# Kernel tuning notes

Hardware: AMD Instinct MI355X
Metric: run time of the kernel (lower is better)

The kernel has to match this reference:

```python
import jax, jax.numpy as jnp
import numpy as np

DIM = 2048
NUM_HEADS = 16
HEAD_DIM = DIM // NUM_HEADS  # 128


def setup_inputs() -> dict:
    key = jax.random.key(0)
    ks = jax.random.split(key, 5)
    scale = 0.02
    x = jax.random.normal(ks[0], (1, 2048, DIM), dtype=jnp.float32)
    # nn.Linear weights stored as [out_features, in_features]
    Wq = jax.random.normal(ks[1], (DIM, DIM), dtype=jnp.float32) * scale
    Wk = jax.random.normal(ks[2], (HEAD_DIM, DIM), dtype=jnp.float32) * scale
    Wv = jax.random.normal(ks[3], (HEAD_DIM, DIM), dtype=jnp.float32) * scale
    Wo = jax.random.normal(ks[4], (DIM, DIM), dtype=jnp.float32) * scale
    return {"x": x, "Wq": Wq, "Wk": Wk, "Wv": Wv, "Wo": Wo}


def reference(x, Wq, Wk, Wv, Wo):
    batch, seq_len, dim = x.shape
    q = x @ Wq.T                                   # [b, s, dim]
    k = x @ Wk.T                                   # [b, s, head_dim] (shared across heads)
    v = x @ Wv.T                                   # [b, s, head_dim]
    q = q.reshape(batch, seq_len, NUM_HEADS, HEAD_DIM).transpose(0, 2, 1, 3)  # [b, h, s, d]
    # MQA: single KV head broadcast across query heads (no materialized repeat)
    scores = jnp.einsum("bhqd,bkd->bhqk", q, k) / (HEAD_DIM ** 0.5)
    probs = jax.nn.softmax(scores, axis=-1)        # [b, h, q, k]
    out = jnp.einsum("bhqk,bkd->bhqd", probs, v)   # [b, h, s, d]
    out = out.transpose(0, 2, 1, 3).reshape(batch, seq_len, dim)
    return out @ Wo.T
```

## Files before the change

kernel.cpp:

```cpp
#include <hip/hip_runtime.h>
#include <cmath>

typedef float  float4_t __attribute__((ext_vector_type(4)));
typedef __bf16 bf16x8   __attribute__((ext_vector_type(8)));
typedef unsigned short u16;

__device__ __forceinline__ u16 f2bf(float f) {
    unsigned u = __float_as_uint(f);
    u += 0x7fffu + ((u >> 16) & 1u);
    return (u16)(u >> 16);
}

#define GLOAD_LDS16(g, l)                                              \
    __builtin_amdgcn_global_load_lds(                                  \
        (__attribute__((address_space(1))) void*)(g),                  \
        (__attribute__((address_space(3))) void*)(l), 16, 0, 0)

__global__ __launch_bounds__(256) void cast_all(const float* __restrict__ x,
                                                const float* __restrict__ wq,
                                                const float* __restrict__ wk,
                                                const float* __restrict__ wv,
                                                const float* __restrict__ wo,
                                                u16* __restrict__ xb, u16* __restrict__ wqb,
                                                u16* __restrict__ wkb, u16* __restrict__ wvb,
                                                u16* __restrict__ wob) {
    const int b = blockIdx.x;
    const float* src;
    u16* dst;
    int i;
    if (b < 4096)      { src = x;  dst = xb;  i = b * 256 + threadIdx.x; }
    else if (b < 8192) { src = wq; dst = wqb; i = (b - 4096) * 256 + threadIdx.x; }
    else if (b < 8448) { src = wk; dst = wkb; i = (b - 8192) * 256 + threadIdx.x; }
    else if (b < 8704) { src = wv; dst = wvb; i = (b - 8448) * 256 + threadIdx.x; }
    else               { src = wo; dst = wob; i = (b - 8704) * 256 + threadIdx.x; }
    float4 f = ((const float4*)src)[i];
    ushort4 r;
    r.x = f2bf(f.x); r.y = f2bf(f.y); r.z = f2bf(f.z); r.w = f2bf(f.w);
    ((ushort4*)dst)[i] = r;
}

template <typename EPI>
__device__ __forceinline__ void gemm_core(const u16* __restrict__ A,
                                          const u16* __restrict__ B,
                                          int K, int bm, int bn, EPI epi) {
    __shared__ __align__(16) u16 As[2 * 64 * 32];
    __shared__ __align__(16) u16 Bs[2 * 128 * 32];
    const int tid  = threadIdx.x;
    const int lane = tid & 63, wave = tid >> 6;
    const int quad = lane >> 4, l16 = lane & 15;

    float4_t acc[4][2] = {};

    for (int k0 = 0; k0 < K; k0 += 64) {
#pragma unroll
        for (int i = 0; i < 2; ++i) {
            const int slot = i * 256 + tid;
            const int ks = slot >> 8, win = slot & 255;
            const int row = win >> 2, ch = (win & 3) * 8;
            GLOAD_LDS16(A + (size_t)(bm + row) * K + k0 + ks * 32 + ch, &As[slot * 8]);
        }
#pragma unroll
        for (int i = 0; i < 4; ++i) {
            const int slot = i * 256 + tid;
            const int ks = slot >> 9, win = slot & 511;
            const int row = win >> 2, ch = (win & 3) * 8;
            GLOAD_LDS16(B + (size_t)(bn + row) * K + k0 + ks * 32 + ch, &Bs[slot * 8]);
        }
        __syncthreads();

        bf16x8 af[2][4], bfr[2][2];
#pragma unroll
        for (int ks = 0; ks < 2; ++ks) {
#pragma unroll
            for (int mi = 0; mi < 4; ++mi)
                af[ks][mi] = *(const bf16x8*)&As[ks * 2048 + (mi * 16 + l16) * 32 + quad * 8];
#pragma unroll
            for (int ni = 0; ni < 2; ++ni)
                bfr[ks][ni] = *(const bf16x8*)&Bs[ks * 4096 + (wave * 32 + ni * 16 + l16) * 32 + quad * 8];
        }
#pragma unroll
        for (int mi = 0; mi < 4; ++mi)
#pragma unroll
            for (int ni = 0; ni < 2; ++ni) {
                acc[mi][ni] = __builtin_amdgcn_mfma_f32_16x16x32_bf16(
                    af[0][mi], bfr[0][ni], acc[mi][ni], 0, 0, 0);
                acc[mi][ni] = __builtin_amdgcn_mfma_f32_16x16x32_bf16(
                    af[1][mi], bfr[1][ni], acc[mi][ni], 0, 0, 0);
            }
        __syncthreads();
    }

#pragma unroll
    for (int mi = 0; mi < 4; ++mi) {
        const int row = bm + mi * 16 + quad * 4;
#pragma unroll
        for (int ni = 0; ni < 2; ++ni) {
            const int col = bn + wave * 32 + ni * 16 + l16;
#pragma unroll
            for (int r = 0; r < 4; ++r) epi(row + r, col, acc[mi][ni][r]);
        }
    }
}

__global__ __launch_bounds__(256) void gemm_qkv(const u16* __restrict__ A,
                                                const u16* __restrict__ B,
                                                u16* __restrict__ qb,
                                                u16* __restrict__ kb,
                                                u16* __restrict__ vtb) {
    gemm_core(A, B, 2048, blockIdx.x * 64, blockIdx.y * 128,
              [=](int row, int col, float v) {
                  if (col < 2048)
                      qb[(size_t)row * 2048 + col] = f2bf(v * 0.1275174313451427f);
                  else if (col < 2176)
                      kb[(size_t)row * 128 + (col - 2048)] = f2bf(v);
                  else
                      vtb[(size_t)(col - 2176) * 2048 + row] = f2bf(v);
              });
}

__global__ __launch_bounds__(256) void gemm_out(const u16* __restrict__ A,
                                                const u16* __restrict__ B,
                                                float* __restrict__ C) {
    gemm_core(A, B, 2048, blockIdx.x * 64, blockIdx.y * 128,
              [=](int row, int col, float v) {
                  C[(size_t)row * 2048 + col] = v;
              });
}

__global__ __launch_bounds__(256) void mqa_attn(const u16* __restrict__ Q,
                                                const u16* __restrict__ Kmat,
                                                const u16* __restrict__ Vt,
                                                float* __restrict__ Oacc0,
                                                float* __restrict__ Oacc1,
                                                float* __restrict__ Lsum) {
    __shared__ __align__(16) u16 Ks[4 * 32 * 32];
    __shared__ __align__(16) u16 Vts[128 * 32];
    __shared__ __align__(16) u16 Ps[4][32 * 40];
    const int tid  = threadIdx.x;
    const int wave = tid >> 6, lane = tid & 63;
    const int quad = lane >> 4, l16 = lane & 15;
    const int h     = blockIdx.y;
    const int ks    = blockIdx.z;
    const int qbase = blockIdx.x * 128 + wave * 32;
    const int kbase = ks * 1024;

    bf16x8 qf[2][4];
#pragma unroll
    for (int mt = 0; mt < 2; ++mt)
#pragma unroll
        for (int kb4 = 0; kb4 < 4; ++kb4)
            qf[mt][kb4] = *(const bf16x8*)(Q + (size_t)(qbase + mt * 16 + l16) * 2048 +
                                           h * 128 + kb4 * 32 + quad * 8);

    float4_t acc[2][8];
#pragma unroll
    for (int mt = 0; mt < 2; ++mt)
#pragma unroll
        for (int nt = 0; nt < 8; ++nt) acc[mt][nt] = (float4_t){0.f, 0.f, 0.f, 0.f};
    float lsum[8] = {};

    u16* pb = Ps[wave];

    for (int s = 0; s < 32; ++s) {
        const int k0 = kbase + s * 32;
#pragma unroll
        for (int i = 0; i < 2; ++i) {
            const int slot = i * 256 + tid;
            const int kb4 = slot >> 7, win = slot & 127;
            const int row = win >> 2, ch = (win & 3) * 8;
            GLOAD_LDS16(Kmat + (size_t)(k0 + row) * 128 + kb4 * 32 + ch, &Ks[slot * 8]);
        }
#pragma unroll
        for (int i = 0; i < 2; ++i) {
            const int slot = i * 256 + tid;
            const int d = slot >> 2, ch = (slot & 3) * 8;
            GLOAD_LDS16(Vt + (size_t)d * 2048 + k0 + ch, &Vts[slot * 8]);
        }
        __syncthreads();

#pragma unroll
        for (int ct = 0; ct < 2; ++ct) {
            float4_t s0 = (float4_t){0.f, 0.f, 0.f, 0.f};
            float4_t s1 = (float4_t){0.f, 0.f, 0.f, 0.f};
#pragma unroll
            for (int kb4 = 0; kb4 < 4; ++kb4) {
                bf16x8 kf = *(const bf16x8*)&Ks[kb4 * 1024 + (ct * 16 + l16) * 32 + quad * 8];
                s0 = __builtin_amdgcn_mfma_f32_16x16x32_bf16(qf[0][kb4], kf, s0, 0, 0, 0);
                s1 = __builtin_amdgcn_mfma_f32_16x16x32_bf16(qf[1][kb4], kf, s1, 0, 0, 0);
            }
#pragma unroll
            for (int r = 0; r < 4; ++r) {
                const float e0 = exp2f(s0[r]);
                const float e1 = exp2f(s1[r]);
                lsum[r]     += e0;
                lsum[4 + r] += e1;
                pb[(quad * 4 + r) * 40 + ct * 16 + l16]      = f2bf(e0);
                pb[(16 + quad * 4 + r) * 40 + ct * 16 + l16] = f2bf(e1);
            }
        }
        bf16x8 pa[2];
#pragma unroll
        for (int mt = 0; mt < 2; ++mt)
            pa[mt] = *(const bf16x8*)&pb[(mt * 16 + l16) * 40 + quad * 8];
#pragma unroll
        for (int nt = 0; nt < 8; ++nt) {
            bf16x8 vf = *(const bf16x8*)&Vts[(nt * 16 + l16) * 32 + quad * 8];
            acc[0][nt] = __builtin_amdgcn_mfma_f32_16x16x32_bf16(pa[0], vf, acc[0][nt], 0, 0, 0);
            acc[1][nt] = __builtin_amdgcn_mfma_f32_16x16x32_bf16(pa[1], vf, acc[1][nt], 0, 0, 0);
        }
        __syncthreads();
    }

    float* __restrict__ Op = ks ? Oacc1 : Oacc0;
#pragma unroll
    for (int mt = 0; mt < 2; ++mt)
#pragma unroll
        for (int r = 0; r < 4; ++r) {
            const int row = qbase + mt * 16 + quad * 4 + r;
            const size_t base = ((size_t)h * 2048 + row) * 128;
            float lrow = lsum[mt * 4 + r];
#pragma unroll
            for (int off = 1; off < 16; off <<= 1) lrow += __shfl_xor(lrow, off);
            if (l16 == 0) Lsum[(size_t)ks * 32768 + h * 2048 + row] = lrow;
#pragma unroll
            for (int nt = 0; nt < 8; ++nt)
                Op[base + nt * 16 + l16] = acc[mt][nt][r];
        }
}

__global__ __launch_bounds__(256) void attn_combine(const float* __restrict__ O0,
                                                    const float* __restrict__ O1,
                                                    const float* __restrict__ L,
                                                    u16* __restrict__ attn) {
    const int f = blockIdx.x * 256 + threadIdx.x;
    const int d4 = f & 31, h = (f >> 5) & 15, q = f >> 9;
    const int li = h * 2048 + q;
    const float inv = 1.0f / (L[li] + L[32768 + li]);
    const int oi = li * 32 + d4;
    const float4 a = ((const float4*)O0)[oi];
    const float4 b = ((const float4*)O1)[oi];
    ushort4 r;
    r.x = f2bf((a.x + b.x) * inv);
    r.y = f2bf((a.y + b.y) * inv);
    r.z = f2bf((a.z + b.z) * inv);
    r.w = f2bf((a.w + b.w) * inv);
    ((ushort4*)attn)[f] = r;
}

extern "C" void kernel_launch(void* const* d_in, const int* in_sizes, int n_in,
                              void* d_out, int out_size, void* d_ws, size_t ws_size,
                              hipStream_t stream) {
    const float* x  = (const float*)d_in[0];
    const float* Wq = (const float*)d_in[1];
    const float* Wk = (const float*)d_in[2];
    const float* Wv = (const float*)d_in[3];
    const float* Wo = (const float*)d_in[4];
    float* out = (float*)d_out;

    u16* ws   = (u16*)d_ws;
    u16* xb   = ws;
    u16* Wqb  = xb  + (4 << 20);
    u16* Wkb  = Wqb + (4 << 20);
    u16* Wvb  = Wkb + (256 << 10);
    u16* Wob  = Wvb + (256 << 10);
    u16* qb   = Wob + (4 << 20);
    u16* kb   = qb  + (4 << 20);
    u16* vtb  = kb  + (256 << 10);
    u16* attn = vtb + (256 << 10);
    float* Oacc0 = (float*)ws;
    float* Oacc1 = (float*)(attn + (4 << 20));
    float* Lsum  = Oacc1 + (4 << 20);

    cast_all<<<12800, 256, 0, stream>>>(x, Wq, Wk, Wv, Wo, xb, Wqb, Wkb, Wvb, Wob);

    gemm_qkv<<<dim3(32, 18), 256, 0, stream>>>(xb, Wqb, qb, kb, vtb);
    mqa_attn<<<dim3(16, 16, 2), 256, 0, stream>>>(qb, kb, vtb, Oacc0, Oacc1, Lsum);
    attn_combine<<<4096, 256, 0, stream>>>(Oacc0, Oacc1, Lsum, attn);
    gemm_out<<<dim3(32, 16), 256, 0, stream>>>(attn, Wob, out);
}
```

Measured before the change: 235.8 us.

## Split-K the GEMMs with 128x128 tiles and split attention keys four ways using atomics

The QKV and output GEMMs now use 128x128 block tiles over a 2x2 wave grid and split K in two across blockIdx.z. Partial results are accumulated with float atomics into zeroed buffers, and a new qkv_combine pass does the bf16 conversion, the Q scaling and the V transpose. Attention splits the key range into four chunks instead of two and accumulates O and the row sums atomically, so attn_combine reads one buffer. The aim is better tile reuse and more blocks in flight. The cost is extra memsets, atomic traffic, an extra elementwise pass and non-deterministic summation order.

```diff
diff --git a/kernel.cpp b/kernel.cpp
--- a/kernel.cpp
+++ b/kernel.cpp
@@ -40,99 +40,110 @@
 }
 
 template <typename EPI>
-__device__ __forceinline__ void gemm_core(const u16* __restrict__ A,
-                                          const u16* __restrict__ B,
-                                          int K, int bm, int bn, EPI epi) {
-    __shared__ __align__(16) u16 As[2 * 64 * 32];
-    __shared__ __align__(16) u16 Bs[2 * 128 * 32];
+__device__ __forceinline__ void gemm128_core(const u16* __restrict__ A,
+                                             const u16* __restrict__ B,
+                                             int ldk, int klen, int bm, int bn, EPI epi) {
+    __shared__ __align__(16) u16 As[128 * 32];
+    __shared__ __align__(16) u16 Bs[128 * 32];
     const int tid  = threadIdx.x;
     const int lane = tid & 63, wave = tid >> 6;
+    const int wm = wave >> 1, wn = wave & 1;
     const int quad = lane >> 4, l16 = lane & 15;
 
-    float4_t acc[4][2] = {};
-
-    for (int k0 = 0; k0 < K; k0 += 64) {
+    float4_t acc[4][4] = {};
+    const int r0 = tid >> 2;
+    const int c0 = (tid & 3) * 8;
+
+    for (int k0 = 0; k0 < klen; k0 += 32) {
 #pragma unroll
         for (int i = 0; i < 2; ++i) {
-            const int slot = i * 256 + tid;
-            const int ks = slot >> 8, win = slot & 255;
-            const int row = win >> 2, ch = (win & 3) * 8;
-            GLOAD_LDS16(A + (size_t)(bm + row) * K + k0 + ks * 32 + ch, &As[slot * 8]);
-        }
-#pragma unroll
-        for (int i = 0; i < 4; ++i) {
-            const int slot = i * 256 + tid;
-            const int ks = slot >> 9, win = slot & 511;
-            const int row = win >> 2, ch = (win & 3) * 8;
-            GLOAD_LDS16(B + (size_t)(bn + row) * K + k0 + ks * 32 + ch, &Bs[slot * 8]);
-        }
-        __syncthreads();
-
-        bf16x8 af[2][4], bfr[2][2];
-#pragma unroll
-        for (int ks = 0; ks < 2; ++ks) {
-#pragma unroll
-            for (int mi = 0; mi < 4; ++mi)
-                af[ks][mi] = *(const bf16x8*)&As[ks * 2048 + (mi * 16 + l16) * 32 + quad * 8];
-#pragma unroll
-            for (int ni = 0; ni < 2; ++ni)
-                bfr[ks][ni] = *(const bf16x8*)&Bs[ks * 4096 + (wave * 32 + ni * 16 + l16) * 32 + quad * 8];
-        }
+            const int row = i * 64 + r0;
+            const int e   = (i * 256 + tid) * 8;
+            GLOAD_LDS16(A + (size_t)(bm + row) * ldk + k0 + c0, &As[e]);
+            GLOAD_LDS16(B + (size_t)(bn + row) * ldk + k0 + c0, &Bs[e]);
+        }
+        __syncthreads();
+
+        bf16x8 af[4], bfr[4];
 #pragma unroll
         for (int mi = 0; mi < 4; ++mi)
-#pragma unroll
-            for (int ni = 0; ni < 2; ++ni) {
+            af[mi] = *(const bf16x8*)&As[(wm * 64 + mi * 16 + l16) * 32 + quad * 8];
+#pragma unroll
+        for (int ni = 0; ni < 4; ++ni)
+            bfr[ni] = *(const bf16x8*)&Bs[(wn * 64 + ni * 16 + l16) * 32 + quad * 8];
+#pragma unroll
+        for (int mi = 0; mi < 4; ++mi)
+#pragma unroll
+            for (int ni = 0; ni < 4; ++ni)
                 acc[mi][ni] = __builtin_amdgcn_mfma_f32_16x16x32_bf16(
-                    af[0][mi], bfr[0][ni], acc[mi][ni], 0, 0, 0);
-                acc[mi][ni] = __builtin_amdgcn_mfma_f32_16x16x32_bf16(
-                    af[1][mi], bfr[1][ni], acc[mi][ni], 0, 0, 0);
-            }
+                    af[mi], bfr[ni], acc[mi][ni], 0, 0, 0);
         __syncthreads();
     }
 
 #pragma unroll
     for (int mi = 0; mi < 4; ++mi) {
-        const int row = bm + mi * 16 + quad * 4;
-#pragma unroll
-        for (int ni = 0; ni < 2; ++ni) {
-            const int col = bn + wave * 32 + ni * 16 + l16;
+        const int row = bm + wm * 64 + mi * 16 + quad * 4;
+#pragma unroll
+        for (int ni = 0; ni < 4; ++ni) {
+            const int col = bn + wn * 64 + ni * 16 + l16;
 #pragma unroll
             for (int r = 0; r < 4; ++r) epi(row + r, col, acc[mi][ni][r]);
         }
     }
 }
 
-__global__ __launch_bounds__(256) void gemm_qkv(const u16* __restrict__ A,
-                                                const u16* __restrict__ B,
-                                                u16* __restrict__ qb,
-                                                u16* __restrict__ kb,
-                                                u16* __restrict__ vtb) {
-    gemm_core(A, B, 2048, blockIdx.x * 64, blockIdx.y * 128,
-              [=](int row, int col, float v) {
-                  if (col < 2048)
-                      qb[(size_t)row * 2048 + col] = f2bf(v * 0.1275174313451427f);
-                  else if (col < 2176)
-                      kb[(size_t)row * 128 + (col - 2048)] = f2bf(v);
-                  else
-                      vtb[(size_t)(col - 2176) * 2048 + row] = f2bf(v);
-              });
-}
-
-__global__ __launch_bounds__(256) void gemm_out(const u16* __restrict__ A,
-                                                const u16* __restrict__ B,
-                                                float* __restrict__ C) {
-    gemm_core(A, B, 2048, blockIdx.x * 64, blockIdx.y * 128,
-              [=](int row, int col, float v) {
-                  C[(size_t)row * 2048 + col] = v;
-              });
-}
-
-__global__ __launch_bounds__(256) void mqa_attn(const u16* __restrict__ Q,
-                                                const u16* __restrict__ Kmat,
-                                                const u16* __restrict__ Vt,
-                                                float* __restrict__ Oacc0,
-                                                float* __restrict__ Oacc1,
-                                                float* __restrict__ Lsum) {
+__global__ __launch_bounds__(256) void gemm_qkv_s(const u16* __restrict__ A,
+                                                  const u16* __restrict__ B,
+                                                  float* __restrict__ Pqkv) {
+    const int z = blockIdx.z;
+    gemm128_core(A + z * 1024, B + z * 1024, 2048, 1024,
+                 blockIdx.x * 128, blockIdx.y * 128,
+                 [=](int row, int col, float v) {
+                     unsafeAtomicAdd(&Pqkv[(size_t)row * 2304 + col], v);
+                 });
+}
+
+__global__ __launch_bounds__(256) void gemm_out_s(const u16* __restrict__ A,
+                                                  const u16* __restrict__ B,
+                                                  float* __restrict__ C) {
+    const int z = blockIdx.z;
+    gemm128_core(A + z * 1024, B + z * 1024, 2048, 1024,
+                 blockIdx.x * 128, blockIdx.y * 128,
+                 [=](int row, int col, float v) {
+                     unsafeAtomicAdd(&C[(size_t)row * 2048 + col], v);
+                 });
+}
+
+__global__ __launch_bounds__(256) void qkv_combine(const float* __restrict__ P,
+                                                   u16* __restrict__ qb,
+                                                   u16* __restrict__ kb,
+                                                   u16* __restrict__ vtb) {
+    const int f = blockIdx.x * 256 + threadIdx.x;
+    const int r = f / 576, c = f % 576;
+    const int col = c * 4;
+    const float4 v = ((const float4*)P)[f];
+    if (col < 2048) {
+        const float s = 0.1275174313451427f;
+        ushort4 o;
+        o.x = f2bf(v.x * s); o.y = f2bf(v.y * s); o.z = f2bf(v.z * s); o.w = f2bf(v.w * s);
+        ((ushort4*)qb)[(r * 2048 + col) >> 2] = o;
+    } else if (col < 2176) {
+        ushort4 o;
+        o.x = f2bf(v.x); o.y = f2bf(v.y); o.z = f2bf(v.z); o.w = f2bf(v.w);
+        ((ushort4*)kb)[(r * 128 + col - 2048) >> 2] = o;
+    } else {
+        vtb[(size_t)(col - 2176 + 0) * 2048 + r] = f2bf(v.x);
+        vtb[(size_t)(col - 2176 + 1) * 2048 + r] = f2bf(v.y);
+        vtb[(size_t)(col - 2176 + 2) * 2048 + r] = f2bf(v.z);
+        vtb[(size_t)(col - 2176 + 3) * 2048 + r] = f2bf(v.w);
+    }
+}
+
+__global__ __launch_bounds__(256, 4) void mqa_attn(const u16* __restrict__ Q,
+                                                   const u16* __restrict__ Kmat,
+                                                   const u16* __restrict__ Vt,
+                                                   float* __restrict__ Oacc,
+                                                   float* __restrict__ Lsum) {
     __shared__ __align__(16) u16 Ks[4 * 32 * 32];
     __shared__ __align__(16) u16 Vts[128 * 32];
     __shared__ __align__(16) u16 Ps[4][32 * 40];
@@ -140,9 +151,8 @@
     const int wave = tid >> 6, lane = tid & 63;
     const int quad = lane >> 4, l16 = lane & 15;
     const int h     = blockIdx.y;
-    const int ks    = blockIdx.z;
     const int qbase = blockIdx.x * 128 + wave * 32;
-    const int kbase = ks * 1024;
+    const int kbase = blockIdx.z * 512;
 
     bf16x8 qf[2][4];
 #pragma unroll
@@ -161,7 +171,7 @@
 
     u16* pb = Ps[wave];
 
-    for (int s = 0; s < 32; ++s) {
+    for (int s = 0; s < 16; ++s) {
         const int k0 = kbase + s * 32;
 #pragma unroll
         for (int i = 0; i < 2; ++i) {
@@ -211,7 +221,6 @@
         __syncthreads();
     }
 
-    float* __restrict__ Op = ks ? Oacc1 : Oacc0;
 #pragma unroll
     for (int mt = 0; mt < 2; ++mt)
 #pragma unroll
@@ -221,29 +230,26 @@
             float lrow = lsum[mt * 4 + r];
 #pragma unroll
             for (int off = 1; off < 16; off <<= 1) lrow += __shfl_xor(lrow, off);
-            if (l16 == 0) Lsum[(size_t)ks * 32768 + h * 2048 + row] = lrow;
+            if (l16 == 0) unsafeAtomicAdd(&Lsum[h * 2048 + row], lrow);
 #pragma unroll
             for (int nt = 0; nt < 8; ++nt)
-                Op[base + nt * 16 + l16] = acc[mt][nt][r];
-        }
-}
-
-__global__ __launch_bounds__(256) void attn_combine(const float* __restrict__ O0,
-                                                    const float* __restrict__ O1,
+                unsafeAtomicAdd(&Oacc[base + nt * 16 + l16], acc[mt][nt][r]);
+        }
+}
+
+__global__ __launch_bounds__(256) void attn_combine(const float* __restrict__ O,
                                                     const float* __restrict__ L,
                                                     u16* __restrict__ attn) {
     const int f = blockIdx.x * 256 + threadIdx.x;
     const int d4 = f & 31, h = (f >> 5) & 15, q = f >> 9;
     const int li = h * 2048 + q;
-    const float inv = 1.0f / (L[li] + L[32768 + li]);
-    const int oi = li * 32 + d4;
-    const float4 a = ((const float4*)O0)[oi];
-    const float4 b = ((const float4*)O1)[oi];
+    const float inv = 1.0f / L[li];
+    const float4 a = ((const float4*)O)[li * 32 + d4];
     ushort4 r;
-    r.x = f2bf((a.x + b.x) * inv);
-    r.y = f2bf((a.y + b.y) * inv);
-    r.z = f2bf((a.z + b.z) * inv);
-    r.w = f2bf((a.w + b.w) * inv);
+    r.x = f2bf(a.x * inv);
+    r.y = f2bf(a.y * inv);
+    r.z = f2bf(a.z * inv);
+    r.w = f2bf(a.w * inv);
     ((ushort4*)attn)[f] = r;
 }
 
@@ -267,14 +273,19 @@
     u16* kb   = qb  + (4 << 20);
     u16* vtb  = kb  + (256 << 10);
     u16* attn = vtb + (256 << 10);
-    float* Oacc0 = (float*)ws;
-    float* Oacc1 = (float*)(attn + (4 << 20));
-    float* Lsum  = Oacc1 + (4 << 20);
+    float* Pqkv = (float*)(attn + (4 << 20));
+    float* Oacc = (float*)ws;
+    float* Lsum = Oacc + (4 << 20);
+
+    hipMemsetAsync(out, 0, (size_t)2048 * 2048 * 4, stream);
+    hipMemsetAsync(Pqkv, 0, (size_t)2048 * 2304 * 4, stream);
 
     cast_all<<<12800, 256, 0, stream>>>(x, Wq, Wk, Wv, Wo, xb, Wqb, Wkb, Wvb, Wob);
 
-    gemm_qkv<<<dim3(32, 18), 256, 0, stream>>>(xb, Wqb, qb, kb, vtb);
-    mqa_attn<<<dim3(16, 16, 2), 256, 0, stream>>>(qb, kb, vtb, Oacc0, Oacc1, Lsum);
-    attn_combine<<<4096, 256, 0, stream>>>(Oacc0, Oacc1, Lsum, attn);
-    gemm_out<<<dim3(32, 16), 256, 0, stream>>>(attn, Wob, out);
-}
+    gemm_qkv_s<<<dim3(16, 18, 2), 256, 0, stream>>>(xb, Wqb, Pqkv);
+    hipMemsetAsync(Oacc, 0, (size_t)(16 << 20) + (128 << 10), stream);
+    qkv_combine<<<4608, 256, 0, stream>>>(Pqkv, qb, kb, vtb);
+    mqa_attn<<<dim3(16, 16, 4), 256, 0, stream>>>(qb, kb, vtb, Oacc, Lsum);
+    attn_combine<<<4096, 256, 0, stream>>>(Oacc, Lsum, attn);
+    gemm_out_s<<<dim3(16, 16, 2), 256, 0, stream>>>(attn, Wob, out);
+}
```

Measured after the change: 405.5 us. 1.72x slower.

## Use 128x128 GEMM tiles, split-K output projection, and tighter P padding

Applied to the files above, without the earlier changes.

The GEMM core moves from 64x128 tiles with a K-step of 64 to 128x128 tiles with a K-step of 32, with the four waves in a 2x2 layout, to raise operand reuse per LDS load. The QKV GEMM grid halves accordingly. The output projection is split along K into two partial GEMMs written to scratch buffers and summed by a new combine kernel, which restores block count but adds an extra fp32 round trip. The attention P tile row stride changes from 40 to 36 to alter LDS bank mapping, so each fragment is now read as two 8-byte loads.

```diff
diff --git a/kernel.cpp b/kernel.cpp
--- a/kernel.cpp
+++ b/kernel.cpp
@@ -3,6 +3,7 @@
 
 typedef float  float4_t __attribute__((ext_vector_type(4)));
 typedef __bf16 bf16x8   __attribute__((ext_vector_type(8)));
+typedef __bf16 bf16x4   __attribute__((ext_vector_type(4)));
 typedef unsigned short u16;
 
 __device__ __forceinline__ u16 f2bf(float f) {
@@ -40,62 +41,52 @@
 }
 
 template <typename EPI>
-__device__ __forceinline__ void gemm_core(const u16* __restrict__ A,
-                                          const u16* __restrict__ B,
-                                          int K, int bm, int bn, EPI epi) {
-    __shared__ __align__(16) u16 As[2 * 64 * 32];
-    __shared__ __align__(16) u16 Bs[2 * 128 * 32];
+__device__ __forceinline__ void gemm128_core(const u16* __restrict__ A,
+                                             const u16* __restrict__ B,
+                                             int ldk, int klen, int bm, int bn, EPI epi) {
+    __shared__ __align__(16) u16 As[128 * 32];
+    __shared__ __align__(16) u16 Bs[128 * 32];
     const int tid  = threadIdx.x;
     const int lane = tid & 63, wave = tid >> 6;
+    const int wm = wave >> 1, wn = wave & 1;
     const int quad = lane >> 4, l16 = lane & 15;
 
-    float4_t acc[4][2] = {};
-
-    for (int k0 = 0; k0 < K; k0 += 64) {
+    float4_t acc[4][4] = {};
+    const int r0 = tid >> 2;
+    const int c0 = (tid & 3) * 8;
+
+    for (int k0 = 0; k0 < klen; k0 += 32) {
 #pragma unroll
         for (int i = 0; i < 2; ++i) {
-            const int slot = i * 256 + tid;
-            const int ks = slot >> 8, win = slot & 255;
-            const int row = win >> 2, ch = (win & 3) * 8;
-            GLOAD_LDS16(A + (size_t)(bm + row) * K + k0 + ks * 32 + ch, &As[slot * 8]);
-        }
-#pragma unroll
-        for (int i = 0; i < 4; ++i) {
-            const int slot = i * 256 + tid;
-            const int ks = slot >> 9, win = slot & 511;
-            const int row = win >> 2, ch = (win & 3) * 8;
-            GLOAD_LDS16(B + (size_t)(bn + row) * K + k0 + ks * 32 + ch, &Bs[slot * 8]);
-        }
-        __syncthreads();
-
-        bf16x8 af[2][4], bfr[2][2];
-#pragma unroll
-        for (int ks = 0; ks < 2; ++ks) {
-#pragma unroll
-            for (int mi = 0; mi < 4; ++mi)
-                af[ks][mi] = *(const bf16x8*)&As[ks * 2048 + (mi * 16 + l16) * 32 + quad * 8];
-#pragma unroll
-            for (int ni = 0; ni < 2; ++ni)
-                bfr[ks][ni] = *(const bf16x8*)&Bs[ks * 4096 + (wave * 32 + ni * 16 + l16) * 32 + quad * 8];
-        }
+            const int row = i * 64 + r0;
+            const int e   = (i * 256 + tid) * 8;
+            GLOAD_LDS16(A + (size_t)(bm + row) * ldk + k0 + c0, &As[e]);
+            GLOAD_LDS16(B + (size_t)(bn + row) * ldk + k0 + c0, &Bs[e]);
+        }
+        __syncthreads();
+
+        bf16x8 af[4], bfr[4];
 #pragma unroll
         for (int mi = 0; mi < 4; ++mi)
-#pragma unroll
-            for (int ni = 0; ni < 2; ++ni) {
+            af[mi] = *(const bf16x8*)&As[(wm * 64 + mi * 16 + l16) * 32 + quad * 8];
+#pragma unroll
+        for (int ni = 0; ni < 4; ++ni)
+            bfr[ni] = *(const bf16x8*)&Bs[(wn * 64 + ni * 16 + l16) * 32 + quad * 8];
+#pragma unroll
+        for (int mi = 0; mi < 4; ++mi)
+#pragma unroll
+            for (int ni = 0; ni < 4; ++ni)
                 acc[mi][ni] = __builtin_amdgcn_mfma_f32_16x16x32_bf16(
-                    af[0][mi], bfr[0][ni], acc[mi][ni], 0, 0, 0);
-                acc[mi][ni] = __builtin_amdgcn_mfma_f32_16x16x32_bf16(
-                    af[1][mi], bfr[1][ni], acc[mi][ni], 0, 0, 0);
-            }
+                    af[mi], bfr[ni], acc[mi][ni], 0, 0, 0);
         __syncthreads();
     }
 
 #pragma unroll
     for (int mi = 0; mi < 4; ++mi) {
-        const int row = bm + mi * 16 + quad * 4;
-#pragma unroll
-        for (int ni = 0; ni < 2; ++ni) {
-            const int col = bn + wave * 32 + ni * 16 + l16;
+        const int row = bm + wm * 64 + mi * 16 + quad * 4;
+#pragma unroll
+        for (int ni = 0; ni < 4; ++ni) {
+            const int col = bn + wn * 64 + ni * 16 + l16;
 #pragma unroll
             for (int r = 0; r < 4; ++r) epi(row + r, col, acc[mi][ni][r]);
         }
@@ -107,24 +98,39 @@
                                                 u16* __restrict__ qb,
                                                 u16* __restrict__ kb,
                                                 u16* __restrict__ vtb) {
-    gemm_core(A, B, 2048, blockIdx.x * 64, blockIdx.y * 128,
-              [=](int row, int col, float v) {
-                  if (col < 2048)
-                      qb[(size_t)row * 2048 + col] = f2bf(v * 0.1275174313451427f);
-                  else if (col < 2176)
-                      kb[(size_t)row * 128 + (col - 2048)] = f2bf(v);
-                  else
-                      vtb[(size_t)(col - 2176) * 2048 + row] = f2bf(v);
-              });
-}
-
-__global__ __launch_bounds__(256) void gemm_out(const u16* __restrict__ A,
-                                                const u16* __restrict__ B,
-                                                float* __restrict__ C) {
-    gemm_core(A, B, 2048, blockIdx.x * 64, blockIdx.y * 128,
-              [=](int row, int col, float v) {
-                  C[(size_t)row * 2048 + col] = v;
-              });
+    gemm128_core(A, B, 2048, 2048, blockIdx.x * 128, blockIdx.y * 128,
+                 [=](int row, int col, float v) {
+                     if (col < 2048)
+                         qb[(size_t)row * 2048 + col] = f2bf(v * 0.1275174313451427f);
+                     else if (col < 2176)
+                         kb[(size_t)row * 128 + (col - 2048)] = f2bf(v);
+                     else
+                         vtb[(size_t)(col - 2176) * 2048 + row] = f2bf(v);
+                 });
+}
+
+__global__ __launch_bounds__(256) void gemm_out_s(const u16* __restrict__ A,
+                                                  const u16* __restrict__ B,
+                                                  float* __restrict__ P0,
+                                                  float* __restrict__ P1) {
+    const int z = blockIdx.z;
+    float* __restrict__ P = z ? P1 : P0;
+    gemm128_core(A + z * 1024, B + z * 1024, 2048, 1024,
+                 blockIdx.x * 128, blockIdx.y * 128,
+                 [=](int row, int col, float v) {
+                     P[(size_t)row * 2048 + col] = v;
+                 });
+}
+
+__global__ __launch_bounds__(256) void out_combine(const float* __restrict__ P0,
+                                                   const float* __restrict__ P1,
+                                                   float* __restrict__ out) {
+    const int f = blockIdx.x * 256 + threadIdx.x;
+    const float4 a = ((const float4*)P0)[f];
+    const float4 b = ((const float4*)P1)[f];
+    float4 r;
+    r.x = a.x + b.x; r.y = a.y + b.y; r.z = a.z + b.z; r.w = a.w + b.w;
+    ((float4*)out)[f] = r;
 }
 
 __global__ __launch_bounds__(256) void mqa_attn(const u16* __restrict__ Q,
@@ -135,7 +141,7 @@
                                                 float* __restrict__ Lsum) {
     __shared__ __align__(16) u16 Ks[4 * 32 * 32];
     __shared__ __align__(16) u16 Vts[128 * 32];
-    __shared__ __align__(16) u16 Ps[4][32 * 40];
+    __shared__ __align__(16) u16 Ps[4][32 * 36];
     const int tid  = threadIdx.x;
     const int wave = tid >> 6, lane = tid & 63;
     const int quad = lane >> 4, l16 = lane & 15;
@@ -194,14 +200,18 @@
                 const float e1 = exp2f(s1[r]);
                 lsum[r]     += e0;
                 lsum[4 + r] += e1;
-                pb[(quad * 4 + r) * 40 + ct * 16 + l16]      = f2bf(e0);
-                pb[(16 + quad * 4 + r) * 40 + ct * 16 + l16] = f2bf(e1);
+                pb[(quad * 4 + r) * 36 + ct * 16 + l16]      = f2bf(e0);
+                pb[(16 + quad * 4 + r) * 36 + ct * 16 + l16] = f2bf(e1);
             }
         }
         bf16x8 pa[2];
 #pragma unroll
-        for (int mt = 0; mt < 2; ++mt)
-            pa[mt] = *(const bf16x8*)&pb[(mt * 16 + l16) * 40 + quad * 8];
+        for (int mt = 0; mt < 2; ++mt) {
+            const int base = (mt * 16 + l16) * 36 + quad * 8;
+            bf16x4 lo = *(const bf16x4*)&pb[base];
+            bf16x4 hi = *(const bf16x4*)&pb[base + 4];
+            pa[mt] = __builtin_shufflevector(lo, hi, 0, 1, 2, 3, 4, 5, 6, 7);
+        }
 #pragma unroll
         for (int nt = 0; nt < 8; ++nt) {
             bf16x8 vf = *(const bf16x8*)&Vts[(nt * 16 + l16) * 32 + quad * 8];
@@ -270,11 +280,14 @@
     float* Oacc0 = (float*)ws;
     float* Oacc1 = (float*)(attn + (4 << 20));
     float* Lsum  = Oacc1 + (4 << 20);
+    float* Po0   = (float*)ws;
+    float* Po1   = Oacc1;
 
     cast_all<<<12800, 256, 0, stream>>>(x, Wq, Wk, Wv, Wo, xb, Wqb, Wkb, Wvb, Wob);
 
-    gemm_qkv<<<dim3(32, 18), 256, 0, stream>>>(xb, Wqb, qb, kb, vtb);
+    gemm_qkv<<<dim3(16, 18), 256, 0, stream>>>(xb, Wqb, qb, kb, vtb);
     mqa_attn<<<dim3(16, 16, 2), 256, 0, stream>>>(qb, kb, vtb, Oacc0, Oacc1, Lsum);
     attn_combine<<<4096, 256, 0, stream>>>(Oacc0, Oacc1, Lsum, attn);
-    gemm_out<<<dim3(32, 16), 256, 0, stream>>>(attn, Wob, out);
-}
+    gemm_out_s<<<dim3(16, 16, 2), 256, 0, stream>>>(attn, Wob, Po0, Po1);
+    out_combine<<<4096, 256, 0, stream>>>(Po0, Po1, out);
+}
```

Result: slower. 254.9 us (+8.1%).
